# Performance work log

Measured on AMD Instinct MI355X. Metric: run time of the kernel, lower is better.

## Reference

```python
import jax, jax.numpy as jnp
import numpy as np

H = 256          # hidden_size
K = 3            # pointer hops
LAMDA = 3.0
EPS = 1e-8       # torch cosine_similarity eps
# dropout is treated as eval-mode (identity)


def _gru_cell(x, h, wi, wh, bi, bh):
    # torch GRUCell: gate order reset, update, new
    gx = x @ wi.T + bi            # (B, 3*4H)
    gh = h @ wh.T + bh
    xr, xz, xn = jnp.split(gx, 3, axis=-1)
    hr, hz, hn = jnp.split(gh, 3, axis=-1)
    r = jax.nn.sigmoid(xr + hr)
    z = jax.nn.sigmoid(xz + hz)
    n = jnp.tanh(xn + r * hn)
    return (1.0 - z) * n + z * h


def setup_inputs() -> dict:
    key = jax.random.key(0)
    ks = jax.random.split(key, 16)
    B, L = 128, 512
    d2, d4 = 2 * H, 4 * H
    sc = lambda i, shape, fan: jax.random.normal(ks[i], shape, jnp.float32) * (1.0 / np.sqrt(fan))
    return {
        "m": jax.random.normal(ks[0], (B, L, d2), jnp.float32),
        "s1": jax.random.normal(ks[1], (B, d4), jnp.float32),
        "s2": jax.random.normal(ks[2], (B, d4), jnp.float32),
        "s3": jax.random.normal(ks[3], (B, d4), jnp.float32),
        "m_mask": jnp.ones((B, L), jnp.int32),
        "w2_w": sc(4, (d2, d2), d2), "w2_b": jnp.zeros((d2,), jnp.float32),
        "w3_w": sc(5, (d4, d2), d4), "w3_b": jnp.zeros((d2,), jnp.float32),
        "w4_w": sc(6, (d4, d4), d4), "w4_b": jnp.zeros((d4,), jnp.float32),
        "w5_w": sc(7, (d4, 1), d4), "w5_b": jnp.zeros((1,), jnp.float32),
        "gru_wi": sc(8, (3 * d4, d2), d2),
        "gru_wh": sc(9, (3 * d4, d4), d4),
        "gru_bi": jnp.zeros((3 * d4,), jnp.float32),
        "gru_bh": jnp.zeros((3 * d4,), jnp.float32),
    }


def reference(m, s1, s2, s3, m_mask,
              w2_w, w2_b, w3_w, w3_b, w4_w, w4_b, w5_w, w5_b,
              gru_wi, gru_wh, gru_bi, gru_bh):
    # m: (B, L, 2H); s*: (B, 4H); m_mask: (B, L)
    mtt = m @ w2_w + w2_b                         # (B, L, 2H), loop-invariant
    m_norm = jnp.maximum(jnp.linalg.norm(mtt, axis=-1), EPS)  # (B, L)
    invalid = m_mask == 0

    def branch(st):
        for _ in range(K):
            stt = st @ w3_w + w3_b                # (B, 2H)
            s_norm = jnp.maximum(jnp.linalg.norm(stt, axis=-1), EPS)  # (B,)
            dot = jnp.einsum('bld,bd->bl', mtt, stt)
            att = LAMDA * dot / (m_norm * s_norm[:, None])
            att = jnp.where(invalid, -jnp.inf, att)
            p = jax.nn.softmax(att, axis=1)       # (B, L)
            f_att = jnp.einsum('bl,bld->bd', p, m)  # (B, 2H)
            st = _gru_cell(f_att, st, gru_wi, gru_wh, gru_bi, gru_bh)
        h = jax.nn.relu(st @ w4_w + w4_b)         # (B, 4H)
        return (h @ w5_w + w5_b)[:, 0]            # (B,)

    result = jnp.stack([branch(s1), branch(s2), branch(s3)], axis=1)  # (B, 3)
    return jax.nn.log_softmax(result, axis=1)
```

## Files before the change

### kernel.cpp

```cpp
#include <hip/hip_runtime.h>
#include <math.h>

constexpr int B  = 128;
constexpr int L  = 512;
constexpr int D2 = 512;
constexpr int D4 = 1024;
constexpr int G3 = 3072;
constexpr int R3 = 384;
constexpr int NC = 4096;
constexpr float LAMDA = 3.0f;
constexpr float EPSF  = 1e-8f;

typedef __attribute__((ext_vector_type(8))) short bf16x8;
typedef __attribute__((ext_vector_type(8))) short short8;
typedef __attribute__((ext_vector_type(4))) float f32x4;

__device__ __forceinline__ ushort f2bf(float v) {
  uint u = __builtin_bit_cast(uint, v);
  u = (u + 0x7fffu + ((u >> 16) & 1u)) >> 16;
  return (ushort)u;
}
__device__ __forceinline__ float bf2f(ushort h) {
  return __builtin_bit_cast(float, (uint)h << 16);
}
__device__ __forceinline__ float bflo(uint w) { return __builtin_bit_cast(float, w << 16); }
__device__ __forceinline__ float bfhi(uint w) { return __builtin_bit_cast(float, w & 0xffff0000u); }
__device__ __forceinline__ void split2(float v, ushort& h, ushort& l) {
  h = f2bf(v);
  l = f2bf(v - bf2f(h));
}

__global__ void k_init(const float* __restrict__ s1, const float* __restrict__ s2,
                       const float* __restrict__ s3, float* __restrict__ st3,
                       ushort* __restrict__ sth, ushort* __restrict__ stl,
                       float* __restrict__ snacc, float* __restrict__ cacc,
                       float* __restrict__ o3) {
  int idx = blockIdx.x * blockDim.x + threadIdx.x;
  if (idx < R3) { snacc[idx] = 0.f; cacc[idx] = 0.f; o3[idx] = 0.f; }
  int total = R3 * D4;
  for (; idx < total; idx += gridDim.x * blockDim.x) {
    int r = idx / D4, i = idx - r * D4;
    int k = r / B, b = r - k * B;
    const float* s = (k == 0) ? s1 : (k == 1) ? s2 : s3;
    float v = s[b * D4 + i];
    st3[idx] = v;
    if (sth) { ushort h, l; split2(v, h, l); sth[idx] = h; stl[idx] = l; }
  }
}

__global__ void k_conv_m(const float* __restrict__ m, ushort* __restrict__ mbf) {
  int idx = blockIdx.x * blockDim.x + threadIdx.x;
  const int total8 = (B * L * D2) / 8;
  for (; idx < total8; idx += gridDim.x * blockDim.x) {
    const float4* p = reinterpret_cast<const float4*>(m) + (size_t)idx * 2;
    float4 a = p[0], c = p[1];
    ushort o[8] = {f2bf(a.x), f2bf(a.y), f2bf(a.z), f2bf(a.w),
                   f2bf(c.x), f2bf(c.y), f2bf(c.z), f2bf(c.w)};
    *reinterpret_cast<uint4*>(mbf + (size_t)idx * 8) = *reinterpret_cast<const uint4*>(o);
  }
}

__global__ void k_w2t(const float* __restrict__ w2, ushort* __restrict__ w2t) {
  __shared__ ushort t[64][65];
  int bk = (blockIdx.x & 7) * 64, bn = (blockIdx.x >> 3) * 64;
  int tid = threadIdx.x;
#pragma unroll
  for (int i = 0; i < 16; ++i) {
    int e = tid + i * 256; int r = e >> 6, c = e & 63;
    t[r][c] = f2bf(w2[(bk + r) * 512 + bn + c]);
  }
  __syncthreads();
#pragma unroll
  for (int i = 0; i < 16; ++i) {
    int e = tid + i * 256; int r = e >> 6, c = e & 63;
    w2t[(bn + r) * 512 + bk + c] = t[c][r];
  }
}

__global__ void k_split_direct(const float* __restrict__ in, ushort* __restrict__ oh,
                               ushort* __restrict__ ol, int n4) {
  int idx = blockIdx.x * blockDim.x + threadIdx.x;
  for (; idx < n4; idx += gridDim.x * blockDim.x) {
    float4 v = reinterpret_cast<const float4*>(in)[idx];
    ushort4 h, l;
    split2(v.x, h.x, l.x); split2(v.y, h.y, l.y);
    split2(v.z, h.z, l.z); split2(v.w, h.w, l.w);
    reinterpret_cast<ushort4*>(oh)[idx] = h;
    reinterpret_cast<ushort4*>(ol)[idx] = l;
  }
}

__global__ void k_split_trans(const float* __restrict__ in, int K, int N,
                              ushort* __restrict__ oh, ushort* __restrict__ ol) {
  __shared__ float t[64][65];
  int bk = blockIdx.x * 64, bn = blockIdx.y * 64;
  int tid = threadIdx.x;
#pragma unroll
  for (int i = 0; i < 16; ++i) {
    int e = tid + i * 256; int r = e >> 6, c = e & 63;
    t[r][c] = in[(size_t)(bk + r) * N + bn + c];
  }
  __syncthreads();
#pragma unroll
  for (int i = 0; i < 16; ++i) {
    int e = tid + i * 256; int r = e >> 6, c = e & 63;
    ushort h, l;
    split2(t[c][r], h, l);
    oh[(size_t)(bn + r) * K + bk + c] = h;
    ol[(size_t)(bn + r) * K + bk + c] = l;
  }
}

__global__ void k_bcat2(const float* __restrict__ w3b, const float* __restrict__ gbh,
                        const float* __restrict__ w2w, float* __restrict__ bcat) {
  int idx = blockIdx.x * 256 + threadIdx.x;
  if (idx < D2) bcat[idx] = w3b[idx];
  else if (idx < D2 + G3) bcat[idx] = gbh[idx - D2];
  else if (idx < NC) {
    int e = idx - (D2 + G3);
    float s = 0.f;
    for (int d = 0; d < D2; ++d) s = fmaf(w3b[d], w2w[(size_t)e * D2 + d], s);
    bcat[idx] = s;
  }
}

__global__ __launch_bounds__(64) void k_gemm_wf(
    const ushort* __restrict__ Ahp, const ushort* __restrict__ Alp,
    const ushort* __restrict__ Bhp, const ushort* __restrict__ Blp,
    ushort* __restrict__ Ch, ushort* __restrict__ Cl) {
  const int ln = threadIdx.x;
  const int lrow = ln & 15, lk = ln >> 4;
  const int rowb = blockIdx.y * 64;
  const int colb = blockIdx.x * 64;
  size_t aoff[4], boff[4];
#pragma unroll
  for (int f = 0; f < 4; ++f) {
    aoff[f] = (size_t)(rowb + f * 16 + lrow) * D2 + lk * 8;
    boff[f] = (size_t)(colb + f * 16 + lrow) * D2 + lk * 8;
  }
  f32x4 acc[4][4] = {};
  for (int kc = 0; kc < D2; kc += 32) {
    bf16x8 ah[4], al[4], bh[4], bl[4];
#pragma unroll
    for (int f = 0; f < 4; ++f) {
      ah[f] = *reinterpret_cast<const bf16x8*>(Ahp + aoff[f] + kc);
      al[f] = *reinterpret_cast<const bf16x8*>(Alp + aoff[f] + kc);
      bh[f] = *reinterpret_cast<const bf16x8*>(Bhp + boff[f] + kc);
      bl[f] = *reinterpret_cast<const bf16x8*>(Blp + boff[f] + kc);
    }
#pragma unroll
    for (int rf = 0; rf < 4; ++rf)
#pragma unroll
      for (int cf = 0; cf < 4; ++cf) {
        acc[rf][cf] = __builtin_amdgcn_mfma_f32_16x16x32_bf16(ah[rf], bh[cf], acc[rf][cf], 0, 0, 0);
        acc[rf][cf] = __builtin_amdgcn_mfma_f32_16x16x32_bf16(al[rf], bh[cf], acc[rf][cf], 0, 0, 0);
        acc[rf][cf] = __builtin_amdgcn_mfma_f32_16x16x32_bf16(ah[rf], bl[cf], acc[rf][cf], 0, 0, 0);
      }
  }
#pragma unroll
  for (int rf = 0; rf < 4; ++rf)
#pragma unroll
    for (int cf = 0; cf < 4; ++cf) {
      int col = colb + cf * 16 + lrow;
#pragma unroll
      for (int j = 0; j < 4; ++j) {
        int row = rowb + rf * 16 + lk * 4 + j;
        ushort h, l;
        split2(acc[rf][cf][j], h, l);
        Ch[(size_t)row * D4 + col] = h;
        Cl[(size_t)row * D4 + col] = l;
      }
    }
}

#define MN_LOAD(AF_, BF_, KC_)                                                              \
  do {                                                                                      \
    _Pragma("unroll") for (int rf = 0; rf < 2; ++rf)                                        \
        AF_[rf] = *reinterpret_cast<const bf16x8*>(ap0 + (size_t)rf * 16 * 512 + (KC_));    \
    _Pragma("unroll") for (int cf = 0; cf < 8; ++cf)                                        \
        BF_[cf] = *reinterpret_cast<const bf16x8*>(bp0 + (size_t)cf * 16 * 512 + (KC_));    \
  } while (0)
#define MN_MFMA(AF_, BF_)                                                                   \
  do {                                                                                      \
    _Pragma("unroll") for (int rf = 0; rf < 2; ++rf)                                        \
        _Pragma("unroll") for (int cf = 0; cf < 8; ++cf)                                    \
            acc[rf][cf] = __builtin_amdgcn_mfma_f32_16x16x32_bf16(AF_[rf], BF_[cf],         \
                                                                  acc[rf][cf], 0, 0, 0);    \
  } while (0)

__global__ __launch_bounds__(256) void k_mnorm3(const ushort* __restrict__ mbf,
                                                const ushort* __restrict__ w2t,
                                                const float* __restrict__ b2,
                                                float* __restrict__ norm2) {
  const int tid = threadIdx.x;
  const int wv = tid >> 6, ln = tid & 63;
  const int lrow = ln & 15, lk = ln >> 4;
  const size_t rowb = (size_t)blockIdx.x * 32;
  const ushort* ap0 = mbf + (rowb + lrow) * 512 + lk * 8;
  const ushort* bp0 = w2t + (size_t)(wv * 128 + lrow) * 512 + lk * 8;
  f32x4 acc[2][8] = {};
  bf16x8 aA[2], bA[8], aB[2], bB[8];
  MN_LOAD(aA, bA, 0);
  for (int kc = 0; kc < 512; kc += 64) {
    MN_LOAD(aB, bB, kc + 32);
    MN_MFMA(aA, bA);
    if (kc + 64 < 512) MN_LOAD(aA, bA, kc + 64);
    MN_MFMA(aB, bB);
  }
  float nrm[2][4] = {};
#pragma unroll
  for (int cf = 0; cf < 8; ++cf) {
    float bb = b2[wv * 128 + cf * 16 + lrow];
#pragma unroll
    for (int rf = 0; rf < 2; ++rf)
#pragma unroll
      for (int j = 0; j < 4; ++j) {
        float v = acc[rf][cf][j] + bb;
        nrm[rf][j] = fmaf(v, v, nrm[rf][j]);
      }
  }
  __shared__ float red[4][32];
#pragma unroll
  for (int rf = 0; rf < 2; ++rf)
#pragma unroll
    for (int j = 0; j < 4; ++j) {
      float v = nrm[rf][j];
      v += __shfl_xor(v, 1); v += __shfl_xor(v, 2);
      v += __shfl_xor(v, 4); v += __shfl_xor(v, 8);
      if (lrow == 0) red[wv][rf * 16 + lk * 4 + j] = v;
    }
  __syncthreads();
  if (tid < 32)
    norm2[rowb + tid] = red[0][tid] + red[1][tid] + red[2][tid] + red[3][tid];
}

#define G3_LOAD(AH_, AL_, BH_, BL_, KC_)                                                    \
  do {                                                                                      \
    _Pragma("unroll") for (int f = 0; f < 2; ++f) {                                         \
      AH_[f] = *reinterpret_cast<const bf16x8*>(ah0 + (size_t)f * 16 * Kd + (KC_));         \
      AL_[f] = *reinterpret_cast<const bf16x8*>(al0 + (size_t)f * 16 * Kd + (KC_));         \
    }                                                                                       \
    _Pragma("unroll") for (int f = 0; f < 4; ++f) {                                         \
      BH_[f] = *reinterpret_cast<const bf16x8*>(bh0 + (size_t)f * 16 * Kd + (KC_));         \
      BL_[f] = *reinterpret_cast<const bf16x8*>(bl0 + (size_t)f * 16 * Kd + (KC_));         \
    }                                                                                       \
  } while (0)
#define G3_MFMA(AH_, AL_, BH_, BL_)                                                         \
  do {                                                                                      \
    _Pragma("unroll") for (int rf = 0; rf < 2; ++rf)                                        \
        _Pragma("unroll") for (int cf = 0; cf < 4; ++cf) {                                  \
      acc[rf][cf] = __builtin_amdgcn_mfma_f32_16x16x32_bf16(AH_[rf], BH_[cf], acc[rf][cf],  \
                                                            0, 0, 0);                       \
      acc[rf][cf] = __builtin_amdgcn_mfma_f32_16x16x32_bf16(AL_[rf], BH_[cf], acc[rf][cf],  \
                                                            0, 0, 0);                       \
      acc[rf][cf] = __builtin_amdgcn_mfma_f32_16x16x32_bf16(AH_[rf], BL_[cf], acc[rf][cf],  \
                                                            0, 0, 0);                       \
    }                                                                                       \
  } while (0)

template <int EPI>
__global__ __launch_bounds__(64) void k_gemm3(
    const ushort* __restrict__ Ahp, const ushort* __restrict__ Alp,
    const ushort* __restrict__ Bhp, const ushort* __restrict__ Blp,
    int Kd, const float* __restrict__ bias,
    float* __restrict__ outf, int ldc,
    float* __restrict__ gh, float* __restrict__ shat,
    float* __restrict__ snacc, float* __restrict__ cacc,
    const float* __restrict__ b2,
    const float* __restrict__ w5w, float* __restrict__ o3) {
  const int ln = threadIdx.x;
  const int lrow = ln & 15, lk = ln >> 4;
  const int rowb = blockIdx.y * 32;
  const int colb = blockIdx.x * 64;
  const ushort* ah0 = Ahp + (size_t)(rowb + lrow) * Kd + lk * 8;
  const ushort* al0 = Alp + (size_t)(rowb + lrow) * Kd + lk * 8;
  const ushort* bh0 = Bhp + (size_t)(colb + lrow) * Kd + lk * 8;
  const ushort* bl0 = Blp + (size_t)(colb + lrow) * Kd + lk * 8;
  f32x4 acc[2][4] = {};
  bf16x8 ahA[2], alA[2], bhA[4], blA[4];
  bf16x8 ahB[2], alB[2], bhB[4], blB[4];
  G3_LOAD(ahA, alA, bhA, blA, 0);
  for (int kc = 0; kc < Kd; kc += 64) {
    G3_LOAD(ahB, alB, bhB, blB, kc + 32);
    G3_MFMA(ahA, alA, bhA, blA);
    if (kc + 64 < Kd) G3_LOAD(ahA, alA, bhA, blA, kc + 64);
    G3_MFMA(ahB, alB, bhB, blB);
  }

  if (EPI == 0) {
#pragma unroll
    for (int rf = 0; rf < 2; ++rf)
#pragma unroll
      for (int cf = 0; cf < 4; ++cf) {
        int col = colb + cf * 16 + lrow;
        float bb = bias ? bias[col] : 0.f;
#pragma unroll
        for (int j = 0; j < 4; ++j) {
          int row = rowb + rf * 16 + lk * 4 + j;
          outf[(size_t)row * ldc + col] = acc[rf][cf][j] + bb;
        }
      }
  } else if (EPI == 1) {
    if (colb < D2) {
      float ss[2][4] = {}, sc[2][4] = {};
#pragma unroll
      for (int cf = 0; cf < 4; ++cf) {
        int col = colb + cf * 16 + lrow;
        float bb = bias[col], bc = b2[col];
#pragma unroll
        for (int rf = 0; rf < 2; ++rf)
#pragma unroll
          for (int j = 0; j < 4; ++j) {
            float v = acc[rf][cf][j] + bb;
            ss[rf][j] = fmaf(v, v, ss[rf][j]);
            sc[rf][j] = fmaf(v, bc, sc[rf][j]);
          }
      }
#pragma unroll
      for (int rf = 0; rf < 2; ++rf)
#pragma unroll
        for (int j = 0; j < 4; ++j) {
          float a = ss[rf][j], c = sc[rf][j];
          a += __shfl_xor(a, 1); c += __shfl_xor(c, 1);
          a += __shfl_xor(a, 2); c += __shfl_xor(c, 2);
          a += __shfl_xor(a, 4); c += __shfl_xor(c, 4);
          a += __shfl_xor(a, 8); c += __shfl_xor(c, 8);
          if (lrow == 0) {
            int row = rowb + rf * 16 + lk * 4 + j;
            atomicAdd(&snacc[row], a);
            atomicAdd(&cacc[row], c);
          }
        }
    } else {
#pragma unroll
      for (int rf = 0; rf < 2; ++rf)
#pragma unroll
        for (int cf = 0; cf < 4; ++cf) {
          int col = colb + cf * 16 + lrow;
          float bb = bias[col];
#pragma unroll
          for (int j = 0; j < 4; ++j) {
            int row = rowb + rf * 16 + lk * 4 + j;
            float v = acc[rf][cf][j] + bb;
            if (colb < D2 + G3) gh[(size_t)row * G3 + (col - D2)] = v;
            else                shat[(size_t)row * D2 + (col - (D2 + G3))] = v;
          }
        }
    }
  } else {
#pragma unroll
    for (int rf = 0; rf < 2; ++rf)
#pragma unroll
      for (int j = 0; j < 4; ++j) {
        float p = 0.f;
#pragma unroll
        for (int cf = 0; cf < 4; ++cf) {
          int col = colb + cf * 16 + lrow;
          float v = fmaxf(acc[rf][cf][j] + bias[col], 0.f);
          p = fmaf(v, w5w[col], p);
        }
        p += __shfl_xor(p, 1); p += __shfl_xor(p, 2);
        p += __shfl_xor(p, 4); p += __shfl_xor(p, 8);
        if (lrow == 0) atomicAdd(&o3[rowb + rf * 16 + lk * 4 + j], p);
      }
  }
}

__global__ __launch_bounds__(256) void k_dot_bf(const ushort* __restrict__ mbf,
                                                const float* __restrict__ shat3,
                                                const float* __restrict__ norm2,
                                                const float* __restrict__ snacc,
                                                const float* __restrict__ cacc,
                                                const int* __restrict__ mask,
                                                float* __restrict__ att3) {
  __shared__ float sh[3][512];
  int b = blockIdx.x >> 3;
  int lt = blockIdx.x & 7;
  int tid = threadIdx.x;
  for (int k = 0; k < 3; ++k)
    for (int i = tid; i < 512; i += 256) sh[k][i] = shat3[(size_t)(k * B + b) * D2 + i];
  __syncthreads();
  int j = tid & 3, lidx = tid >> 2;
  int l = lt * 64 + lidx;
  const uint4* mrow = reinterpret_cast<const uint4*>(mbf + (size_t)(b * L + l) * D2);
  float a0 = 0.f, a1 = 0.f, a2 = 0.f;
#pragma unroll 4
  for (int s = 0; s < 16; ++s) {
    int c = s * 4 + j;
    uint4 mv = mrow[c];
    const float* p0 = &sh[0][c * 8];
    const float* p1 = &sh[1][c * 8];
    const float* p2 = &sh[2][c * 8];
    uint w[4] = {mv.x, mv.y, mv.z, mv.w};
#pragma unroll
    for (int q = 0; q < 4; ++q) {
      float lo = bflo(w[q]), hi = bfhi(w[q]);
      a0 = fmaf(lo, p0[q * 2], a0); a0 = fmaf(hi, p0[q * 2 + 1], a0);
      a1 = fmaf(lo, p1[q * 2], a1); a1 = fmaf(hi, p1[q * 2 + 1], a1);
      a2 = fmaf(lo, p2[q * 2], a2); a2 = fmaf(hi, p2[q * 2 + 1], a2);
    }
  }
  a0 += __shfl_xor(a0, 1); a0 += __shfl_xor(a0, 2);
  a1 += __shfl_xor(a1, 1); a1 += __shfl_xor(a1, 2);
  a2 += __shfl_xor(a2, 1); a2 += __shfl_xor(a2, 2);
  if (j == 0) {
    float mn = fmaxf(sqrtf(norm2[b * L + l]), EPSF);
    bool inv = (mask[b * L + l] == 0);
    float ar[3] = {a0, a1, a2};
#pragma unroll
    for (int k = 0; k < 3; ++k) {
      int r = k * B + b;
      float sn = fmaxf(sqrtf(snacc[r]), EPSF);
      float att = LAMDA * (ar[k] + cacc[r]) / (mn * sn);
      att3[(size_t)r * L + l] = inv ? -INFINITY : att;
    }
  }
}

__global__ void k_softmax(float* __restrict__ att3) {
  int r = blockIdx.x;
  float* row = att3 + (size_t)r * L;
  int tid = threadIdx.x;
  float x0 = row[tid], x1 = row[tid + 256];
  float mx = fmaxf(x0, x1);
  for (int o = 32; o; o >>= 1) mx = fmaxf(mx, __shfl_xor(mx, o));
  __shared__ float rm[4], rs[4];
  int w = tid >> 6;
  if ((tid & 63) == 0) rm[w] = mx;
  __syncthreads();
  mx = fmaxf(fmaxf(rm[0], rm[1]), fmaxf(rm[2], rm[3]));
  float e0 = expf(x0 - mx), e1 = expf(x1 - mx);
  float s = e0 + e1;
  for (int o = 32; o; o >>= 1) s += __shfl_xor(s, o);
  if ((tid & 63) == 0) rs[w] = s;
  __syncthreads();
  s = rs[0] + rs[1] + rs[2] + rs[3];
  float inv = 1.0f / s;
  row[tid] = e0 * inv;
  row[tid + 256] = e1 * inv;
}

__global__ __launch_bounds__(256) void k_fatt_bf(const ushort* __restrict__ mbf,
                                                 const float* __restrict__ p3,
                                                 ushort* __restrict__ fatth,
                                                 ushort* __restrict__ fattl) {
  __shared__ float pp[3][512];
  __shared__ float red[3][256];
  int b = blockIdx.x >> 1, dt = blockIdx.x & 1;
  int tid = threadIdx.x;
  for (int k = 0; k < 3; ++k)
    for (int i = tid; i < 512; i += 256) pp[k][i] = p3[(size_t)(k * B + b) * L + i];
  __syncthreads();
  int dpair = tid & 127, half = tid >> 7;
  int d = dt * 256 + dpair * 2;
  float a[3][2] = {};
  int l0 = half * 256;
#pragma unroll 4
  for (int l = l0; l < l0 + 256; ++l) {
    uint w = *reinterpret_cast<const uint*>(&mbf[(size_t)(b * L + l) * D2 + d]);
    float f0 = bflo(w), f1 = bfhi(w);
#pragma unroll
    for (int k = 0; k < 3; ++k) {
      float p = pp[k][l];
      a[k][0] = fmaf(p, f0, a[k][0]);
      a[k][1] = fmaf(p, f1, a[k][1]);
    }
  }
  if (half == 1) {
#pragma unroll
    for (int k = 0; k < 3; ++k) { red[k][dpair * 2] = a[k][0]; red[k][dpair * 2 + 1] = a[k][1]; }
  }
  __syncthreads();
  if (half == 0) {
#pragma unroll
    for (int k = 0; k < 3; ++k) {
      float v0 = a[k][0] + red[k][dpair * 2];
      float v1 = a[k][1] + red[k][dpair * 2 + 1];
      ushort h0, l0u, h1, l1u;
      split2(v0, h0, l0u); split2(v1, h1, l1u);
      size_t o = (size_t)(k * B + b) * D2 + d;
      fatth[o] = h0;     fattl[o] = l0u;
      fatth[o + 1] = h1; fattl[o + 1] = l1u;
    }
  }
}

__global__ void k_gates(const float* __restrict__ gx, const float* __restrict__ gh,
                        float* __restrict__ st3,
                        ushort* __restrict__ sth, ushort* __restrict__ stl,
                        float* __restrict__ snacc, float* __restrict__ cacc) {
  int idx = blockIdx.x * blockDim.x + threadIdx.x;
  if (snacc && idx < R3) { snacc[idx] = 0.f; cacc[idx] = 0.f; }
  if (idx >= R3 * D4) return;
  int r = idx / D4, i = idx - r * D4;
  const float* gxr = gx + (size_t)r * G3;
  const float* ghr = gh + (size_t)r * G3;
  float xr = gxr[i], xz = gxr[D4 + i], xn = gxr[2 * D4 + i];
  float hr = ghr[i], hz = ghr[D4 + i], hn = ghr[2 * D4 + i];
  float rr = 1.f / (1.f + expf(-(xr + hr)));
  float zz = 1.f / (1.f + expf(-(xz + hz)));
  float nn = tanhf(xn + rr * hn);
  float h = st3[idx];
  float nv = (1.f - zz) * nn + zz * h;
  st3[idx] = nv;
  if (sth) { ushort hh, ll; split2(nv, hh, ll); sth[idx] = hh; stl[idx] = ll; }
}

__global__ void k_final(const float* __restrict__ o3, const float* __restrict__ w5b,
                        float* __restrict__ out) {
  int b = threadIdx.x;
  if (b >= B) return;
  float v0 = o3[0 * B + b] + w5b[0];
  float v1 = o3[1 * B + b] + w5b[0];
  float v2 = o3[2 * B + b] + w5b[0];
  float mx = fmaxf(v0, fmaxf(v1, v2));
  float s = expf(v0 - mx) + expf(v1 - mx) + expf(v2 - mx);
  float lse = mx + logf(s);
  out[b * 3 + 0] = v0 - lse;
  out[b * 3 + 1] = v1 - lse;
  out[b * 3 + 2] = v2 - lse;
}

__global__ __launch_bounds__(256) void k_mnorm(const float* __restrict__ m,
                                               const float* __restrict__ w2,
                                               const float* __restrict__ b2,
                                               float* __restrict__ norm2) {
  __shared__ float As[64][33];
  __shared__ float Ws[32][65];
  __shared__ float red[16][64];
  const int tid = threadIdx.x;
  const int ty = tid >> 4, tx = tid & 15;
  const long rowb = (long)blockIdx.x * 64;
  float rowpart[4] = {0.f, 0.f, 0.f, 0.f};
  for (int ct = 0; ct < 8; ++ct) {
    float acc[4][4] = {};
    for (int kc = 0; kc < 16; ++kc) {
#pragma unroll
      for (int i = 0; i < 8; ++i) {
        int li = tid + i * 256;
        int r = li >> 5, c = li & 31;
        As[r][c] = m[(rowb + r) * 512 + kc * 32 + c];
      }
#pragma unroll
      for (int i = 0; i < 8; ++i) {
        int li = tid + i * 256;
        int r = li >> 6, c = li & 63;
        Ws[r][c] = w2[(kc * 32 + r) * 512 + ct * 64 + c];
      }
      __syncthreads();
#pragma unroll
      for (int k = 0; k < 32; ++k) {
        float a[4], bb[4];
#pragma unroll
        for (int i = 0; i < 4; ++i) a[i] = As[ty * 4 + i][k];
#pragma unroll
        for (int jj = 0; jj < 4; ++jj) bb[jj] = Ws[k][tx * 4 + jj];
#pragma unroll
        for (int i = 0; i < 4; ++i)
#pragma unroll
          for (int jj = 0; jj < 4; ++jj) acc[i][jj] = fmaf(a[i], bb[jj], acc[i][jj]);
      }
      __syncthreads();
    }
#pragma unroll
    for (int jj = 0; jj < 4; ++jj) {
      float bj = b2[ct * 64 + tx * 4 + jj];
#pragma unroll
      for (int i = 0; i < 4; ++i) {
        float v = acc[i][jj] + bj;
        rowpart[i] = fmaf(v, v, rowpart[i]);
      }
    }
  }
#pragma unroll
  for (int i = 0; i < 4; ++i) red[tx][ty * 4 + i] = rowpart[i];
  __syncthreads();
  if (tid < 64) {
    float s = 0.f;
#pragma unroll
    for (int t = 0; t < 16; ++t) s += red[t][tid];
    norm2[rowb + tid] = s;
  }
}

template <bool BT, int ACT>
__global__ __launch_bounds__(256) void k_gemm64(const float* __restrict__ A, int lda,
                                                const float* __restrict__ Bm, int ldb,
                                                const float* __restrict__ bias,
                                                float* __restrict__ C, int ldc, int Kd) {
  __shared__ float As[64][33];
  __shared__ float Bs[32][65];
  const int tid = threadIdx.x;
  const int ty = tid >> 4, tx = tid & 15;
  const int rowb = blockIdx.y * 64;
  const int colb = blockIdx.x * 64;
  float acc[4][4] = {};
  for (int kc = 0; kc < Kd; kc += 32) {
#pragma unroll
    for (int i = 0; i < 8; ++i) {
      int li = tid + i * 256;
      int r = li >> 5, c = li & 31;
      As[r][c] = A[(long)(rowb + r) * lda + kc + c];
    }
    if (!BT) {
#pragma unroll
      for (int i = 0; i < 8; ++i) {
        int li = tid + i * 256;
        int r = li >> 6, c = li & 63;
        Bs[r][c] = Bm[(long)(kc + r) * ldb + colb + c];
      }
    } else {
#pragma unroll
      for (int i = 0; i < 8; ++i) {
        int li = tid + i * 256;
        int n = li >> 5, k = li & 31;
        Bs[k][n] = Bm[(long)(colb + n) * ldb + kc + k];
      }
    }
    __syncthreads();
#pragma unroll
    for (int k = 0; k < 32; ++k) {
      float a[4], bb[4];
#pragma unroll
      for (int i = 0; i < 4; ++i) a[i] = As[ty * 4 + i][k];
#pragma unroll
      for (int jj = 0; jj < 4; ++jj) bb[jj] = Bs[k][tx * 4 + jj];
#pragma unroll
      for (int i = 0; i < 4; ++i)
#pragma unroll
        for (int jj = 0; jj < 4; ++jj) acc[i][jj] = fmaf(a[i], bb[jj], acc[i][jj]);
    }
    __syncthreads();
  }
#pragma unroll
  for (int i = 0; i < 4; ++i) {
    int row = rowb + ty * 4 + i;
#pragma unroll
    for (int jj = 0; jj < 4; ++jj) {
      int col = colb + tx * 4 + jj;
      float v = acc[i][jj];
      if (bias) v += bias[col];
      if (ACT == 1) v = fmaxf(v, 0.f);
      C[(long)row * ldc + col] = v;
    }
  }
}

__global__ void k_snorm(const float* __restrict__ stt3, const float* __restrict__ b2,
                        float* __restrict__ sn3, float* __restrict__ c3) {
  int r = blockIdx.x;
  int tid = threadIdx.x;
  float ss = 0.f, sc = 0.f;
  for (int j = tid; j < D2; j += 256) {
    float v = stt3[(size_t)r * D2 + j];
    ss = fmaf(v, v, ss);
    sc = fmaf(v, b2[j], sc);
  }
  for (int o = 32; o; o >>= 1) {
    ss += __shfl_down(ss, o);
    sc += __shfl_down(sc, o);
  }
  __shared__ float rs[4], rc[4];
  int w = tid >> 6;
  if ((tid & 63) == 0) { rs[w] = ss; rc[w] = sc; }
  __syncthreads();
  if (tid == 0) {
    sn3[r] = fmaxf(sqrtf(rs[0] + rs[1] + rs[2] + rs[3]), EPSF) *
             fmaxf(sqrtf(rs[0] + rs[1] + rs[2] + rs[3]), EPSF) > 0 ?
             fmaxf(sqrtf(rs[0] + rs[1] + rs[2] + rs[3]), EPSF) : EPSF;
    sn3[r] = fmaxf(sqrtf(rs[0] + rs[1] + rs[2] + rs[3]), EPSF);
    c3[r] = rc[0] + rc[1] + rc[2] + rc[3];
  }
}

__global__ __launch_bounds__(256) void k_dot(const float* __restrict__ m,
                                             const float* __restrict__ shat3,
                                             const float* __restrict__ norm2,
                                             const float* __restrict__ sn3,
                                             const float* __restrict__ c3,
                                             const int* __restrict__ mask,
                                             float* __restrict__ att3) {
  __shared__ float sh[3][512];
  int b = blockIdx.x >> 3;
  int lt = blockIdx.x & 7;
  int tid = threadIdx.x;
  for (int k = 0; k < 3; ++k)
    for (int i = tid; i < 512; i += 256) sh[k][i] = shat3[(size_t)(k * B + b) * D2 + i];
  __syncthreads();
  int j = tid & 3, lidx = tid >> 2;
  int l = lt * 64 + lidx;
  const float4* mrow = reinterpret_cast<const float4*>(m + (size_t)(b * L + l) * D2);
  float a0 = 0.f, a1 = 0.f, a2 = 0.f;
#pragma unroll 8
  for (int s = 0; s < 32; ++s) {
    int d4 = s * 4 + j;
    float4 mv = mrow[d4];
    const float4 v0 = *reinterpret_cast<const float4*>(&sh[0][d4 * 4]);
    const float4 v1 = *reinterpret_cast<const float4*>(&sh[1][d4 * 4]);
    const float4 v2 = *reinterpret_cast<const float4*>(&sh[2][d4 * 4]);
    a0 += mv.x * v0.x + mv.y * v0.y + mv.z * v0.z + mv.w * v0.w;
    a1 += mv.x * v1.x + mv.y * v1.y + mv.z * v1.z + mv.w * v1.w;
    a2 += mv.x * v2.x + mv.y * v2.y + mv.z * v2.z + mv.w * v2.w;
  }
  a0 += __shfl_xor(a0, 1); a0 += __shfl_xor(a0, 2);
  a1 += __shfl_xor(a1, 1); a1 += __shfl_xor(a1, 2);
  a2 += __shfl_xor(a2, 1); a2 += __shfl_xor(a2, 2);
  if (j == 0) {
    float mn = fmaxf(sqrtf(norm2[b * L + l]), EPSF);
    bool inv = (mask[b * L + l] == 0);
    float ar[3] = {a0, a1, a2};
#pragma unroll
    for (int k = 0; k < 3; ++k) {
      int r = k * B + b;
      float att = LAMDA * (ar[k] + c3[r]) / (mn * sn3[r]);
      att3[(size_t)r * L + l] = inv ? -INFINITY : att;
    }
  }
}

__global__ __launch_bounds__(256) void k_fatt(const float* __restrict__ m,
                                              const float* __restrict__ p3,
                                              float* __restrict__ fatt3) {
  __shared__ float pp[3][512];
  __shared__ float red[3][128];
  int b = blockIdx.x >> 2, dt = blockIdx.x & 3;
  int tid = threadIdx.x;
  for (int k = 0; k < 3; ++k)
    for (int i = tid; i < 512; i += 256) pp[k][i] = p3[(size_t)(k * B + b) * L + i];
  __syncthreads();
  int d = dt * 128 + (tid & 127);
  int half = tid >> 7;
  float a0 = 0.f, a1 = 0.f, a2 = 0.f;
  int l0 = half * 256;
  for (int l = l0; l < l0 + 256; ++l) {
    float mv = m[(size_t)(b * L + l) * D2 + d];
    a0 = fmaf(pp[0][l], mv, a0);
    a1 = fmaf(pp[1][l], mv, a1);
    a2 = fmaf(pp[2][l], mv, a2);
  }
  int dd = tid & 127;
  if (half == 1) { red[0][dd] = a0; red[1][dd] = a1; red[2][dd] = a2; }
  __syncthreads();
  if (half == 0) {
    fatt3[(size_t)(0 * B + b) * D2 + d] = a0 + red[0][dd];
    fatt3[(size_t)(1 * B + b) * D2 + d] = a1 + red[1][dd];
    fatt3[(size_t)(2 * B + b) * D2 + d] = a2 + red[2][dd];
  }
}

__global__ void k_w5(const float* __restrict__ h4, const float* __restrict__ w5w,
                     float* __restrict__ o3) {
  int r = blockIdx.x, tid = threadIdx.x;
  float s = 0.f;
  for (int d = tid; d < D4; d += 256) s = fmaf(h4[(size_t)r * D4 + d], w5w[d], s);
  for (int o = 32; o; o >>= 1) s += __shfl_down(s, o);
  __shared__ float rs[4];
  if ((tid & 63) == 0) rs[tid >> 6] = s;
  __syncthreads();
  if (tid == 0) o3[r] = rs[0] + rs[1] + rs[2] + rs[3];
}

extern "C" void kernel_launch(void* const* d_in, const int* in_sizes, int n_in,
                              void* d_out, int out_size, void* d_ws, size_t ws_size,
                              hipStream_t stream) {
  const float* m    = (const float*)d_in[0];
  const float* s1   = (const float*)d_in[1];
  const float* s2   = (const float*)d_in[2];
  const float* s3   = (const float*)d_in[3];
  const int*   mask = (const int*)d_in[4];
  const float* w2w  = (const float*)d_in[5];
  const float* w2b  = (const float*)d_in[6];
  const float* w3w  = (const float*)d_in[7];
  const float* w3b  = (const float*)d_in[8];
  const float* w4w  = (const float*)d_in[9];
  const float* w4b  = (const float*)d_in[10];
  const float* w5w  = (const float*)d_in[11];
  const float* w5b  = (const float*)d_in[12];
  const float* gwi  = (const float*)d_in[13];
  const float* gwh  = (const float*)d_in[14];
  const float* gbi  = (const float*)d_in[15];
  const float* gbh  = (const float*)d_in[16];
  float* out = (float*)d_out;

  float* ws = (float*)d_ws;
  size_t off = 0;
  auto alloc = [&](size_t n) {
    float* p = ws + off;
    off += (n + 63) & ~(size_t)63;
    return p;
  };
  ushort* mbf   = (ushort*)alloc((size_t)B * L * D2 / 2);
  ushort* w2t   = (ushort*)alloc((size_t)D2 * D2 / 2);
  ushort* catBh = (ushort*)alloc((size_t)NC * D4 / 2);
  ushort* catBl = (ushort*)alloc((size_t)NC * D4 / 2);
  ushort* gxBh  = (ushort*)alloc((size_t)G3 * D2 / 2);
  ushort* gxBl  = (ushort*)alloc((size_t)G3 * D2 / 2);
  ushort* w4Bh  = (ushort*)alloc((size_t)D4 * D4 / 2);
  ushort* w4Bl  = (ushort*)alloc((size_t)D4 * D4 / 2);
  float* bcat   = alloc(NC);
  float* norm2  = alloc((size_t)B * L);
  float* st3    = alloc((size_t)R3 * D4);
  ushort* sth   = (ushort*)alloc((size_t)R3 * D4 / 2);
  ushort* stl   = (ushort*)alloc((size_t)R3 * D4 / 2);
  float* shat3  = alloc((size_t)R3 * D2);
  float* snacc  = alloc(R3);
  float* cacc   = alloc(R3);
  float* o3     = alloc(R3);
  ushort* fatth = (ushort*)alloc((size_t)R3 * D2 / 2);
  ushort* fattl = (ushort*)alloc((size_t)R3 * D2 / 2);
  float* att3   = alloc((size_t)R3 * L);
  float* gx     = alloc((size_t)R3 * G3);
  float* gh     = alloc((size_t)R3 * G3);
  const size_t big_need = off;
  const bool big = ws_size >= big_need * sizeof(float);

  if (big) {
    ushort* w2dh = (ushort*)gh;
    ushort* w2dl = w2dh + (size_t)D2 * D2;
    ushort* w3dh = (ushort*)gx;
    ushort* w3dl = w3dh + (size_t)D4 * D2;

    k_init<<<1536, 256, 0, stream>>>(s1, s2, s3, st3, sth, stl, snacc, cacc, o3);
    k_conv_m<<<2048, 256, 0, stream>>>(m, mbf);
    k_w2t<<<64, 256, 0, stream>>>(w2w, w2t);
    k_mnorm3<<<(B * L) / 32, 256, 0, stream>>>(mbf, w2t, w2b, norm2);
    k_split_trans<<<dim3(D4 / 64, D2 / 64), 256, 0, stream>>>(w3w, D4, D2, catBh, catBl);
    k_split_direct<<<1024, 256, 0, stream>>>(gwh, catBh + (size_t)D2 * D4, catBl + (size_t)D2 * D4,
                                             (G3 * D4) / 4);
    k_split_direct<<<512, 256, 0, stream>>>(gwi, gxBh, gxBl, (G3 * D2) / 4);
    k_split_trans<<<dim3(D4 / 64, D4 / 64), 256, 0, stream>>>(w4w, D4, D4, w4Bh, w4Bl);
    k_split_direct<<<256, 256, 0, stream>>>(w2w, w2dh, w2dl, (D2 * D2) / 4);
    k_split_direct<<<256, 256, 0, stream>>>(w3w, w3dh, w3dl, (D4 * D2) / 4);
    k_bcat2<<<16, 256, 0, stream>>>(w3b, gbh, w2w, bcat);
    k_gemm_wf<<<dim3(D4 / 64, D2 / 64), 64, 0, stream>>>(
        w2dh, w2dl, w3dh, w3dl,
        catBh + (size_t)(D2 + G3) * D4, catBl + (size_t)(D2 + G3) * D4);

    for (int hop = 0; hop < 3; ++hop) {
      k_gemm3<1><<<dim3(NC / 64, R3 / 32), 64, 0, stream>>>(
          sth, stl, catBh, catBl, D4, bcat, nullptr, 0,
          gh, shat3, snacc, cacc, w2b, nullptr, nullptr);
      k_dot_bf<<<B * 8, 256, 0, stream>>>(mbf, shat3, norm2, snacc, cacc, mask, att3);
      k_softmax<<<3 * B, 256, 0, stream>>>(att3);
      k_fatt_bf<<<B * 2, 256, 0, stream>>>(mbf, att3, fatth, fattl);
      k_gemm3<0><<<dim3(G3 / 64, R3 / 32), 64, 0, stream>>>(
          fatth, fattl, gxBh, gxBl, D2, gbi, gx, G3,
          nullptr, nullptr, nullptr, nullptr, nullptr, nullptr, nullptr);
      k_gates<<<1536, 256, 0, stream>>>(gx, gh, st3, sth, stl, snacc, cacc);
    }
    k_gemm3<2><<<dim3(D4 / 64, R3 / 32), 64, 0, stream>>>(
        sth, stl, w4Bh, w4Bl, D4, w4b, nullptr, 0,
        nullptr, nullptr, nullptr, nullptr, nullptr, w5w, o3);
    k_final<<<1, 128, 0, stream>>>(o3, w5b, out);
  } else {
    off = 0;
    float* f_st3   = alloc((size_t)R3 * D4);
    float* f_norm2 = alloc((size_t)B * L);
    float* f_stt   = alloc((size_t)R3 * D2);
    float* f_shat  = alloc((size_t)R3 * D2);
    float* f_sn    = alloc(R3);
    float* f_c     = alloc(R3);
    float* f_att   = alloc((size_t)R3 * L);
    float* f_fatt  = alloc((size_t)R3 * D2);
    float* f_gx    = alloc((size_t)R3 * G3);
    float* f_gh    = alloc((size_t)R3 * G3);
    float* f_h4    = alloc((size_t)R3 * D4);
    float* f_o3    = alloc(R3);
    k_init<<<1536, 256, 0, stream>>>(s1, s2, s3, f_st3, nullptr, nullptr, f_sn, f_c, f_o3);
    k_mnorm<<<(B * L) / 64, 256, 0, stream>>>(m, w2w, w2b, f_norm2);
    for (int hop = 0; hop < 3; ++hop) {
      k_gemm64<false, 0><<<dim3(D2 / 64, R3 / 64), 256, 0, stream>>>(f_st3, D4, w3w, D2, w3b, f_stt, D2, D4);
      k_snorm<<<R3, 256, 0, stream>>>(f_stt, w2b, f_sn, f_c);
      k_gemm64<true, 0><<<dim3(D2 / 64, R3 / 64), 256, 0, stream>>>(f_stt, D2, w2w, D2, nullptr, f_shat, D2, D2);
      k_dot<<<B * 8, 256, 0, stream>>>(m, f_shat, f_norm2, f_sn, f_c, mask, f_att);
      k_softmax<<<3 * B, 256, 0, stream>>>(f_att);
      k_fatt<<<B * 4, 256, 0, stream>>>(m, f_att, f_fatt);
      k_gemm64<true, 0><<<dim3(G3 / 64, R3 / 64), 256, 0, stream>>>(f_fatt, D2, gwi, D2, gbi, f_gx, G3, D2);
      k_gemm64<true, 0><<<dim3(G3 / 64, R3 / 64), 256, 0, stream>>>(f_st3, D4, gwh, D4, gbh, f_gh, G3, D4);
      k_gates<<<1536, 256, 0, stream>>>(f_gx, f_gh, f_st3, nullptr, nullptr, nullptr, nullptr);
    }
    k_gemm64<false, 1><<<dim3(D4 / 64, R3 / 64), 256, 0, stream>>>(f_st3, D4, w4w, D4, w4b, f_h4, D4, D4);
    k_w5<<<R3, 256, 0, stream>>>(f_h4, w5w, f_o3);
    k_final<<<1, 128, 0, stream>>>(f_o3, w5b, out);
  }
}
```

Baseline: 571.4 us.

## Stage m-norm GEMM tiles through swizzled LDS with async global-to-LDS loads

Rewrites the loop-invariant mtt norm GEMM to use 64-row tiles instead of 32, staging A and B tiles into double-buffered, XOR-swizzled shared memory with direct global-to-LDS loads. Previously each wave loaded its B fragments straight from global memory, so W2 was reloaded many times per block. The new version shares B across waves and doubles the A rows handled per block, which cuts global traffic per MFMA. In exchange it uses about 68KB of LDS per block, lowers occupancy, and adds a barrier every k-step. A redundant duplicate store in the s-norm kernel is also removed.

```diff
diff --git a/kernel.cpp b/kernel.cpp
--- a/kernel.cpp
+++ b/kernel.cpp
@@ -28,6 +28,11 @@
 __device__ __forceinline__ void split2(float v, ushort& h, ushort& l) {
   h = f2bf(v);
   l = f2bf(v - bf2f(h));
+}
+__device__ __forceinline__ void gload_lds16(const void* g, void* l) {
+  __builtin_amdgcn_global_load_lds(
+      (const __attribute__((address_space(1))) unsigned int*)g,
+      (__attribute__((address_space(3))) unsigned int*)l, 16, 0, 0);
 }
 
 __global__ void k_init(const float* __restrict__ s1, const float* __restrict__ s2,
@@ -173,55 +178,74 @@
     }
 }
 
-#define MN_LOAD(AF_, BF_, KC_)                                                              \
-  do {                                                                                      \
-    _Pragma("unroll") for (int rf = 0; rf < 2; ++rf)                                        \
-        AF_[rf] = *reinterpret_cast<const bf16x8*>(ap0 + (size_t)rf * 16 * 512 + (KC_));    \
-    _Pragma("unroll") for (int cf = 0; cf < 8; ++cf)                                        \
-        BF_[cf] = *reinterpret_cast<const bf16x8*>(bp0 + (size_t)cf * 16 * 512 + (KC_));    \
-  } while (0)
-#define MN_MFMA(AF_, BF_)                                                                   \
-  do {                                                                                      \
-    _Pragma("unroll") for (int rf = 0; rf < 2; ++rf)                                        \
-        _Pragma("unroll") for (int cf = 0; cf < 8; ++cf)                                    \
-            acc[rf][cf] = __builtin_amdgcn_mfma_f32_16x16x32_bf16(AF_[rf], BF_[cf],         \
-                                                                  acc[rf][cf], 0, 0, 0);    \
-  } while (0)
-
-__global__ __launch_bounds__(256) void k_mnorm3(const ushort* __restrict__ mbf,
-                                                const ushort* __restrict__ w2t,
-                                                const float* __restrict__ b2,
-                                                float* __restrict__ norm2) {
+__global__ __launch_bounds__(256, 2) void k_mnorm4(const ushort* __restrict__ mbf,
+                                                   const ushort* __restrict__ w2t,
+                                                   const float* __restrict__ b2,
+                                                   float* __restrict__ norm2) {
+  __shared__ ushort As[2][64 * 32];
+  __shared__ ushort Bs[2][512 * 32];
   const int tid = threadIdx.x;
   const int wv = tid >> 6, ln = tid & 63;
   const int lrow = ln & 15, lk = ln >> 4;
-  const size_t rowb = (size_t)blockIdx.x * 32;
-  const ushort* ap0 = mbf + (rowb + lrow) * 512 + lk * 8;
-  const ushort* bp0 = w2t + (size_t)(wv * 128 + lrow) * 512 + lk * 8;
-  f32x4 acc[2][8] = {};
-  bf16x8 aA[2], bA[8], aB[2], bB[8];
-  MN_LOAD(aA, bA, 0);
-  for (int kc = 0; kc < 512; kc += 64) {
-    MN_LOAD(aB, bB, kc + 32);
-    MN_MFMA(aA, bA);
-    if (kc + 64 < 512) MN_LOAD(aA, bA, kc + 64);
-    MN_MFMA(aB, bB);
-  }
-  float nrm[2][4] = {};
+  const size_t rowb = (size_t)blockIdx.x * 64;
+
+  auto stage = [&](int buf, int kc) {
+    {
+      int li = wv * 64 + ln;
+      int row = li >> 2, slot = li & 3;
+      const ushort* src = mbf + (rowb + row) * 512 + kc + ((slot ^ (row & 3)) << 3);
+      gload_lds16(src, &As[buf][(size_t)wv * 64 * 8]);
+    }
+#pragma unroll
+    for (int i = 0; i < 8; ++i) {
+      int c = wv * 8 + i;
+      int li = c * 64 + ln;
+      int col = li >> 2, slot = li & 3;
+      const ushort* src = w2t + (size_t)col * 512 + kc + ((slot ^ (col & 3)) << 3);
+      gload_lds16(src, &Bs[buf][(size_t)c * 64 * 8]);
+    }
+  };
+
+  f32x4 acc[4][8] = {};
+  stage(0, 0);
+  __syncthreads();
+  for (int t = 0; t < 16; ++t) {
+    int cur = t & 1;
+    if (t + 1 < 16) stage(cur ^ 1, (t + 1) * 32);
+    bf16x8 af[4], bfr[8];
+#pragma unroll
+    for (int rf = 0; rf < 4; ++rf) {
+      int row = rf * 16 + lrow;
+      af[rf] = *reinterpret_cast<const bf16x8*>(&As[cur][row * 32 + ((lk ^ (row & 3)) << 3)]);
+    }
+#pragma unroll
+    for (int cf = 0; cf < 8; ++cf) {
+      int col = wv * 128 + cf * 16 + lrow;
+      bfr[cf] = *reinterpret_cast<const bf16x8*>(&Bs[cur][col * 32 + ((lk ^ (col & 3)) << 3)]);
+    }
+#pragma unroll
+    for (int rf = 0; rf < 4; ++rf)
+#pragma unroll
+      for (int cf = 0; cf < 8; ++cf)
+        acc[rf][cf] = __builtin_amdgcn_mfma_f32_16x16x32_bf16(af[rf], bfr[cf], acc[rf][cf], 0, 0, 0);
+    __syncthreads();
+  }
+
+  float nrm[4][4] = {};
 #pragma unroll
   for (int cf = 0; cf < 8; ++cf) {
     float bb = b2[wv * 128 + cf * 16 + lrow];
 #pragma unroll
-    for (int rf = 0; rf < 2; ++rf)
+    for (int rf = 0; rf < 4; ++rf)
 #pragma unroll
       for (int j = 0; j < 4; ++j) {
         float v = acc[rf][cf][j] + bb;
         nrm[rf][j] = fmaf(v, v, nrm[rf][j]);
       }
   }
-  __shared__ float red[4][32];
-#pragma unroll
-  for (int rf = 0; rf < 2; ++rf)
+  __shared__ float red[4][64];
+#pragma unroll
+  for (int rf = 0; rf < 4; ++rf)
 #pragma unroll
     for (int j = 0; j < 4; ++j) {
       float v = nrm[rf][j];
@@ -230,7 +254,7 @@
       if (lrow == 0) red[wv][rf * 16 + lk * 4 + j] = v;
     }
   __syncthreads();
-  if (tid < 32)
+  if (tid < 64)
     norm2[rowb + tid] = red[0][tid] + red[1][tid] + red[2][tid] + red[3][tid];
 }
 
@@ -665,9 +689,6 @@
   if ((tid & 63) == 0) { rs[w] = ss; rc[w] = sc; }
   __syncthreads();
   if (tid == 0) {
-    sn3[r] = fmaxf(sqrtf(rs[0] + rs[1] + rs[2] + rs[3]), EPSF) *
-             fmaxf(sqrtf(rs[0] + rs[1] + rs[2] + rs[3]), EPSF) > 0 ?
-             fmaxf(sqrtf(rs[0] + rs[1] + rs[2] + rs[3]), EPSF) : EPSF;
     sn3[r] = fmaxf(sqrtf(rs[0] + rs[1] + rs[2] + rs[3]), EPSF);
     c3[r] = rc[0] + rc[1] + rc[2] + rc[3];
   }
@@ -823,7 +844,7 @@
     k_init<<<1536, 256, 0, stream>>>(s1, s2, s3, st3, sth, stl, snacc, cacc, o3);
     k_conv_m<<<2048, 256, 0, stream>>>(m, mbf);
     k_w2t<<<64, 256, 0, stream>>>(w2w, w2t);
-    k_mnorm3<<<(B * L) / 32, 256, 0, stream>>>(mbf, w2t, w2b, norm2);
+    k_mnorm4<<<(B * L) / 64, 256, 0, stream>>>(mbf, w2t, w2b, norm2);
     k_split_trans<<<dim3(D4 / 64, D2 / 64), 256, 0, stream>>>(w3w, D4, D2, catBh, catBl);
     k_split_direct<<<1024, 256, 0, stream>>>(gwh, catBh + (size_t)D2 * D4, catBl + (size_t)D2 * D4,
                                              (G3 * D4) / 4);
```

Measured after the change: 479.3 us. 16.1% less time.
